# Performance work log

Hardware: AMD Instinct MI355X
Metric: run time of the kernel (lower is better)

Reference implementation:

```python
import jax, jax.numpy as jnp
import numpy as np

# E2M1 (FP4) representable magnitudes and rounding midpoints
LEVELS = jnp.array([0.0, 0.5, 1.0, 1.5, 2.0, 3.0, 4.0, 6.0], dtype=jnp.float32)
BOUNDS = jnp.array([0.25, 0.75, 1.25, 1.75, 2.5, 3.5, 5.0], dtype=jnp.float32)
E2M1_MAX = 6.0
EPS = 1e-12


def e2m1_block_quant_dequant(x, block_size):
    """Block-wise E2M1 fake-quantization along the last dim.

    Per block of `block_size` elements: scale = absmax / 6.0, then
    round-to-nearest onto the E2M1 grid {0,.5,1,1.5,2,3,4,6} (signed)
    and dequantize. Returns (dequantized x, per-block scales).
    """
    shape = x.shape
    nb = shape[-1] // block_size
    xb = x.reshape(*shape[:-1], nb, block_size)
    amax = jnp.max(jnp.abs(xb), axis=-1, keepdims=True)          # [..., nb, 1]
    scale = jnp.maximum(amax / E2M1_MAX, EPS)
    v = xb / scale
    mag = jnp.abs(v)
    # nearest E2M1 level: count how many rounding boundaries |v| exceeds
    idx = jnp.sum((mag[..., None] > BOUNDS).astype(jnp.int32), axis=-1)
    q = jnp.sign(v) * LEVELS[idx] * scale                        # dequantized
    return q.reshape(shape), scale[..., 0]


def setup_inputs() -> dict:
    key = jax.random.key(0)
    k1, k2, k3 = jax.random.split(key, 3)
    x = jax.random.normal(k1, (8, 1500, 1280), dtype=jnp.float32)
    weight = jax.random.normal(k2, (5120, 1280), dtype=jnp.float32) * 0.02
    bias = jax.random.normal(k3, (5120,), dtype=jnp.float32) * 0.01
    return {"x": x, "weight": weight, "bias": bias}


def reference(x, weight, bias):
    # activation quant (block_size_act = 32, along feature dim)
    x_q, _ = e2m1_block_quant_dequant(x, 32)
    # weight quant (block_size_w = 32, along in_features dim)
    w_q, scale_w = e2m1_block_quant_dequant(weight, 32)
    # F.linear: x @ W^T + b
    out = jnp.einsum('bsi,oi->bso', x_q, w_q) + bias
    return (out, scale_w)
```

## Files before the change

kernel.cpp:

```cpp
#include <hip/hip_runtime.h>
#include <hip/hip_fp16.h>


typedef _Float16 f16;
typedef _Float16 f16x8 __attribute__((ext_vector_type(8)));
typedef float f32x4 __attribute__((ext_vector_type(4)));

#define M_ROWS 12000
#define M_PAD  12032
#define N_COLS 5120
#define K_DIM  1280
#define KB     40
#define NT     20
#define NTN    20

#define BAR()   asm volatile("s_barrier" ::: "memory")
#define LGKM0() asm volatile("s_waitcnt lgkmcnt(0)" ::: "memory")
#define GLDS(gp, lp) __builtin_amdgcn_global_load_lds( \
    (const __attribute__((address_space(1))) unsigned*)(gp), \
    (__attribute__((address_space(3))) unsigned*)(lp), 16, 0, 0)

__device__ __forceinline__ float e2m1_level(float a) {
    float lv;
    if (a > 2.5f)       lv = (a > 3.5f) ? ((a > 5.0f) ? 6.0f : 4.0f) : 3.0f;
    else if (a > 1.25f) lv = (a > 1.75f) ? 2.0f : 1.5f;
    else                lv = (a > 0.75f) ? 1.0f : ((a > 0.25f) ? 0.5f : 0.0f);
    return lv;
}

__global__ __launch_bounds__(256) void quant_x_kernel(const float* __restrict__ x,
                                                      f16* __restrict__ xq) {
    int t = blockIdx.x * blockDim.x + threadIdx.x;
    int row = t / 160;
    int c8  = t % 160;
    f16x8 o;
    if (row < M_ROWS) {
        const float* p = x + (size_t)row * K_DIM + c8 * 8;
        float v[8];
        *(float4*)&v[0] = *(const float4*)p;
        *(float4*)&v[4] = *(const float4*)(p + 4);
        float am = 0.0f;
        #pragma unroll
        for (int i = 0; i < 8; ++i) am = fmaxf(am, fabsf(v[i]));
        am = fmaxf(am, __shfl_xor(am, 1));
        am = fmaxf(am, __shfl_xor(am, 2));
        float scale = fmaxf(am / 6.0f, 1e-12f);
        #pragma unroll
        for (int i = 0; i < 8; ++i) {
            float tq = v[i] / scale;
            float q  = copysignf(e2m1_level(fabsf(tq)), tq) * scale;
            o[i] = (f16)q;
        }
    } else {
        #pragma unroll
        for (int i = 0; i < 8; ++i) o[i] = (f16)0.0f;
    }
    *(f16x8*)(xq + (size_t)row * K_DIM + c8 * 8) = o;
}

__global__ __launch_bounds__(256) void quant_w_kernel(const float* __restrict__ w,
                                                      f16* __restrict__ wq,
                                                      float* __restrict__ scale_out) {
    int t = blockIdx.x * blockDim.x + threadIdx.x;
    int row = t / 160;
    int c8  = t % 160;
    const float* p = w + (size_t)row * K_DIM + c8 * 8;
    float v[8];
    *(float4*)&v[0] = *(const float4*)p;
    *(float4*)&v[4] = *(const float4*)(p + 4);
    float am = 0.0f;
    #pragma unroll
    for (int i = 0; i < 8; ++i) am = fmaxf(am, fabsf(v[i]));
    am = fmaxf(am, __shfl_xor(am, 1));
    am = fmaxf(am, __shfl_xor(am, 2));
    float scale = fmaxf(am / 6.0f, 1e-12f);
    if ((t & 3) == 0) scale_out[row * KB + (c8 >> 2)] = scale;
    f16x8 o;
    #pragma unroll
    for (int i = 0; i < 8; ++i) {
        float tq = v[i] / scale;
        float q  = copysignf(e2m1_level(fabsf(tq)), tq) * scale;
        o[i] = (f16)q;
    }
    *(f16x8*)(wq + (size_t)row * K_DIM + c8 * 8) = o;
}


__device__ __forceinline__ void stage_half(const f16* __restrict__ g, f16* l, int tid) {
    #pragma unroll
    for (int s = 0; s < 2; ++s) {
        int j = s * 512 + tid;
        int r = j >> 3;
        int c = (j & 7) ^ (r & 7);
        GLDS(g + (size_t)r * K_DIM + c * 8, l + (size_t)j * 8);
    }
}

template<bool STAGE, int VMN>
__device__ __forceinline__ void tile_body(f16* Ab, f16* Bb,
                                          const f16* gA2, const f16* gB2,
                                          f32x4 (&acc)[8][4],
                                          int tid, int l15, const int (&swz)[2],
                                          int wr, int wc) {
    f16x8 a0[4][2], a1[4][2], b0[2][2], b1[2][2];
    const int arow0 = wr * 128 + l15;
    const int brow0 = wc * 64 + l15;

    #pragma unroll
    for (int fm = 0; fm < 4; ++fm) {
        a0[fm][0] = *(const f16x8*)&Ab[(arow0 + fm * 16) * 64 + swz[0]];
        a0[fm][1] = *(const f16x8*)&Ab[(arow0 + fm * 16) * 64 + swz[1]];
    }
    #pragma unroll
    for (int fn = 0; fn < 2; ++fn) {
        b0[fn][0] = *(const f16x8*)&Bb[(brow0 + fn * 16) * 64 + swz[0]];
        b0[fn][1] = *(const f16x8*)&Bb[(brow0 + fn * 16) * 64 + swz[1]];
    }
    #pragma unroll
    for (int fn = 0; fn < 2; ++fn) {
        b1[fn][0] = *(const f16x8*)&Bb[(brow0 + 32 + fn * 16) * 64 + swz[0]];
        b1[fn][1] = *(const f16x8*)&Bb[(brow0 + 32 + fn * 16) * 64 + swz[1]];
    }
    BAR();
    __builtin_amdgcn_s_setprio(1);
    #pragma unroll
    for (int fm = 0; fm < 4; ++fm)
        #pragma unroll
        for (int fn = 0; fn < 2; ++fn) {
            acc[fm][fn] = __builtin_amdgcn_mfma_f32_16x16x32_f16(a0[fm][0], b0[fn][0], acc[fm][fn], 0, 0, 0);
            acc[fm][fn] = __builtin_amdgcn_mfma_f32_16x16x32_f16(a0[fm][1], b0[fn][1], acc[fm][fn], 0, 0, 0);
        }
    __builtin_amdgcn_s_setprio(0);
    BAR();

    __builtin_amdgcn_s_setprio(1);
    #pragma unroll
    for (int fm = 0; fm < 4; ++fm)
        #pragma unroll
        for (int fn = 0; fn < 2; ++fn) {
            acc[fm][fn + 2] = __builtin_amdgcn_mfma_f32_16x16x32_f16(a0[fm][0], b1[fn][0], acc[fm][fn + 2], 0, 0, 0);
            acc[fm][fn + 2] = __builtin_amdgcn_mfma_f32_16x16x32_f16(a0[fm][1], b1[fn][1], acc[fm][fn + 2], 0, 0, 0);
        }
    __builtin_amdgcn_s_setprio(0);
    LGKM0();
    BAR();

    #pragma unroll
    for (int fm = 0; fm < 4; ++fm) {
        a1[fm][0] = *(const f16x8*)&Ab[(arow0 + 64 + fm * 16) * 64 + swz[0]];
        a1[fm][1] = *(const f16x8*)&Ab[(arow0 + 64 + fm * 16) * 64 + swz[1]];
    }
    if (STAGE) {
        stage_half(gB2, Bb, tid);
        stage_half(gB2 + 128 * K_DIM, Bb + 8192, tid);
    }
    BAR();
    __builtin_amdgcn_s_setprio(1);
    #pragma unroll
    for (int fm = 0; fm < 4; ++fm)
        #pragma unroll
        for (int fn = 0; fn < 2; ++fn) {
            acc[fm + 4][fn + 2] = __builtin_amdgcn_mfma_f32_16x16x32_f16(a1[fm][0], b1[fn][0], acc[fm + 4][fn + 2], 0, 0, 0);
            acc[fm + 4][fn + 2] = __builtin_amdgcn_mfma_f32_16x16x32_f16(a1[fm][1], b1[fn][1], acc[fm + 4][fn + 2], 0, 0, 0);
        }
    __builtin_amdgcn_s_setprio(0);
    LGKM0();
    BAR();

    if (STAGE) {
        stage_half(gA2, Ab, tid);
        stage_half(gA2 + 128 * K_DIM, Ab + 8192, tid);
    }
    BAR();
    __builtin_amdgcn_s_setprio(1);
    #pragma unroll
    for (int fm = 0; fm < 4; ++fm)
        #pragma unroll
        for (int fn = 0; fn < 2; ++fn) {
            acc[fm + 4][fn] = __builtin_amdgcn_mfma_f32_16x16x32_f16(a1[fm][0], b0[fn][0], acc[fm + 4][fn], 0, 0, 0);
            acc[fm + 4][fn] = __builtin_amdgcn_mfma_f32_16x16x32_f16(a1[fm][1], b0[fn][1], acc[fm + 4][fn], 0, 0, 0);
        }
    __builtin_amdgcn_s_setprio(0);
    if (VMN == 8)      asm volatile("s_waitcnt vmcnt(8)" ::: "memory");
    else if (VMN == 0) asm volatile("s_waitcnt vmcnt(0)" ::: "memory");
    BAR();
}

__global__ __launch_bounds__(512, 2) void gemm_kernel(const f16* __restrict__ A,
                                                      const f16* __restrict__ B,
                                                      const float* __restrict__ bias,
                                                      float* __restrict__ C) {
    extern __shared__ f16 sm[];
    int mt = blockIdx.x / NTN;
    int nt = blockIdx.x % NTN;

    int tid  = threadIdx.x;
    int lane = tid & 63;
    int wid  = tid >> 6;
    int wr   = wid >> 2;
    int wc   = wid & 3;
    int l15  = lane & 15;

    int swz[2] = { (((lane >> 4)    ) ^ (lane & 7)) * 8,
                   (((lane >> 4) + 4) ^ (lane & 7)) * 8 };

    const f16* gAb = A + (size_t)(mt * 256) * K_DIM;
    const f16* gBb = B + (size_t)(nt * 256) * K_DIM;

    f16* A0 = sm;
    f16* B0 = sm + 16384;
    f16* A1 = sm + 32768;
    f16* B1 = sm + 49152;

    f32x4 acc[8][4] = {};

    stage_half(gAb,                A0, tid);
    stage_half(gAb + 128 * K_DIM,  A0 + 8192, tid);
    stage_half(gBb,                B0, tid);
    stage_half(gBb + 128 * K_DIM,  B0 + 8192, tid);
    stage_half(gAb + 64,               A1, tid);
    stage_half(gAb + 64 + 128 * K_DIM, A1 + 8192, tid);
    stage_half(gBb + 64,               B1, tid);
    stage_half(gBb + 64 + 128 * K_DIM, B1 + 8192, tid);
    asm volatile("s_waitcnt vmcnt(8)" ::: "memory");
    BAR();

    #pragma unroll 2
    for (int t = 0; t < NT - 2; ++t) {
        f16* Ab = (t & 1) ? A1 : A0;
        f16* Bb = (t & 1) ? B1 : B0;
        tile_body<true, 8>(Ab, Bb, gAb + (t + 2) * 64, gBb + (t + 2) * 64,
                           acc, tid, l15, swz, wr, wc);
    }
    tile_body<false, 0>(A0, B0, gAb, gBb, acc, tid, l15, swz, wr, wc);
    tile_body<false, -1>(A1, B1, gAb, gBb, acc, tid, l15, swz, wr, wc);

    int crow0 = mt * 256 + wr * 128;
    int ccol  = nt * 256 + wc * 64 + l15;
    float bz[4];
    #pragma unroll
    for (int fn = 0; fn < 4; ++fn) bz[fn] = bias[ccol + fn * 16];

    #pragma unroll
    for (int fm = 0; fm < 8; ++fm) {
        #pragma unroll
        for (int j = 0; j < 4; ++j) {
            int row = crow0 + fm * 16 + (lane >> 4) * 4 + j;
            if (row < M_ROWS) {
                float* cp = C + (size_t)row * N_COLS + ccol;
                #pragma unroll
                for (int fn = 0; fn < 4; ++fn)
                    cp[fn * 16] = acc[fm][fn][j] + bz[fn];
            }
        }
    }
}

extern "C" void kernel_launch(void* const* d_in, const int* in_sizes, int n_in,
                              void* d_out, int out_size, void* d_ws, size_t ws_size,
                              hipStream_t stream) {
    const float* x      = (const float*)d_in[0];
    const float* weight = (const float*)d_in[1];
    const float* bias   = (const float*)d_in[2];
    float* out     = (float*)d_out;
    float* scale_w = (float*)d_out + (size_t)M_ROWS * N_COLS;

    f16* xq = (f16*)d_ws;
    f16* wq = (f16*)((char*)d_ws + (size_t)M_PAD * K_DIM * sizeof(f16));

    (void)hipFuncSetAttribute((const void*)gemm_kernel,
                              hipFuncAttributeMaxDynamicSharedMemorySize, 131072);

    {
        int threads = M_PAD * (K_DIM / 8);
        quant_x_kernel<<<threads / 256, 256, 0, stream>>>(x, xq);
    }
    {
        int threads = N_COLS * (K_DIM / 8);
        quant_w_kernel<<<threads / 256, 256, 0, stream>>>(weight, wq, scale_w);
    }
    {
        int grid = (M_PAD / 256) * (N_COLS / 256);
        gemm_kernel<<<grid, 512, 131072, stream>>>(xq, wq, bias, out);
    }
}
```

Before: 209.8 us.

## Prefetch next tile's LDS fragments into registers and cut barriers per K-tile

Restructures the GEMM main loop so the A0/B0 fragments for the next K-tile are read from LDS into a double-buffered register set at the end of the current tile. MFMA blocks now interleave with LDS reads without barriers between them. Staging of both A and B for tile t+2 is merged into one point after a single barrier, which lowers barriers per tile from about six to two. The cost is more VGPR pressure from the doubled fragment registers, which could cause spills or limit occupancy under launch_bounds(512,2).

```diff
diff --git a/kernel.cpp b/kernel.cpp
--- a/kernel.cpp
+++ b/kernel.cpp
@@ -96,65 +96,54 @@
     }
 }
 
-template<bool STAGE, int VMN>
-__device__ __forceinline__ void tile_body(f16* Ab, f16* Bb,
+template<int PAR, bool STAGE, int VM, bool READNEXT>
+__device__ __forceinline__ void tile_body(f16* Xa, f16* Xb,
+                                          const f16* Na, const f16* Nb,
                                           const f16* gA2, const f16* gB2,
+                                          f16x8 (&a0)[2][4][2], f16x8 (&b0)[2][2][2],
                                           f32x4 (&acc)[8][4],
-                                          int tid, int l15, const int (&swz)[2],
-                                          int wr, int wc) {
-    f16x8 a0[4][2], a1[4][2], b0[2][2], b1[2][2];
-    const int arow0 = wr * 128 + l15;
-    const int brow0 = wc * 64 + l15;
+                                          int tid, int arow0, int brow0,
+                                          const int (&swz)[2]) {
+    f16x8 b1[2][2], a1[4][2];
+
+    #pragma unroll
+    for (int fn = 0; fn < 2; ++fn) {
+        b1[fn][0] = *(const f16x8*)&Xb[(brow0 + 32 + fn * 16) * 64 + swz[0]];
+        b1[fn][1] = *(const f16x8*)&Xb[(brow0 + 32 + fn * 16) * 64 + swz[1]];
+    }
+    __builtin_amdgcn_s_setprio(1);
+    #pragma unroll
+    for (int fm = 0; fm < 4; ++fm)
+        #pragma unroll
+        for (int fn = 0; fn < 2; ++fn) {
+            acc[fm][fn] = __builtin_amdgcn_mfma_f32_16x16x32_f16(a0[PAR][fm][0], b0[PAR][fn][0], acc[fm][fn], 0, 0, 0);
+            acc[fm][fn] = __builtin_amdgcn_mfma_f32_16x16x32_f16(a0[PAR][fm][1], b0[PAR][fn][1], acc[fm][fn], 0, 0, 0);
+        }
+    __builtin_amdgcn_s_setprio(0);
 
     #pragma unroll
     for (int fm = 0; fm < 4; ++fm) {
-        a0[fm][0] = *(const f16x8*)&Ab[(arow0 + fm * 16) * 64 + swz[0]];
-        a0[fm][1] = *(const f16x8*)&Ab[(arow0 + fm * 16) * 64 + swz[1]];
-    }
-    #pragma unroll
-    for (int fn = 0; fn < 2; ++fn) {
-        b0[fn][0] = *(const f16x8*)&Bb[(brow0 + fn * 16) * 64 + swz[0]];
-        b0[fn][1] = *(const f16x8*)&Bb[(brow0 + fn * 16) * 64 + swz[1]];
-    }
-    #pragma unroll
-    for (int fn = 0; fn < 2; ++fn) {
-        b1[fn][0] = *(const f16x8*)&Bb[(brow0 + 32 + fn * 16) * 64 + swz[0]];
-        b1[fn][1] = *(const f16x8*)&Bb[(brow0 + 32 + fn * 16) * 64 + swz[1]];
-    }
-    BAR();
-    __builtin_amdgcn_s_setprio(1);
-    #pragma unroll
-    for (int fm = 0; fm < 4; ++fm)
-        #pragma unroll
-        for (int fn = 0; fn < 2; ++fn) {
-            acc[fm][fn] = __builtin_amdgcn_mfma_f32_16x16x32_f16(a0[fm][0], b0[fn][0], acc[fm][fn], 0, 0, 0);
-            acc[fm][fn] = __builtin_amdgcn_mfma_f32_16x16x32_f16(a0[fm][1], b0[fn][1], acc[fm][fn], 0, 0, 0);
-        }
-    __builtin_amdgcn_s_setprio(0);
-    BAR();
-
-    __builtin_amdgcn_s_setprio(1);
-    #pragma unroll
-    for (int fm = 0; fm < 4; ++fm)
-        #pragma unroll
-        for (int fn = 0; fn < 2; ++fn) {
-            acc[fm][fn + 2] = __builtin_amdgcn_mfma_f32_16x16x32_f16(a0[fm][0], b1[fn][0], acc[fm][fn + 2], 0, 0, 0);
-            acc[fm][fn + 2] = __builtin_amdgcn_mfma_f32_16x16x32_f16(a0[fm][1], b1[fn][1], acc[fm][fn + 2], 0, 0, 0);
-        }
-    __builtin_amdgcn_s_setprio(0);
-    LGKM0();
-    BAR();
-
-    #pragma unroll
-    for (int fm = 0; fm < 4; ++fm) {
-        a1[fm][0] = *(const f16x8*)&Ab[(arow0 + 64 + fm * 16) * 64 + swz[0]];
-        a1[fm][1] = *(const f16x8*)&Ab[(arow0 + 64 + fm * 16) * 64 + swz[1]];
-    }
+        a1[fm][0] = *(const f16x8*)&Xa[(arow0 + 64 + fm * 16) * 64 + swz[0]];
+        a1[fm][1] = *(const f16x8*)&Xa[(arow0 + 64 + fm * 16) * 64 + swz[1]];
+    }
+    __builtin_amdgcn_s_setprio(1);
+    #pragma unroll
+    for (int fm = 0; fm < 4; ++fm)
+        #pragma unroll
+        for (int fn = 0; fn < 2; ++fn) {
+            acc[fm][fn + 2] = __builtin_amdgcn_mfma_f32_16x16x32_f16(a0[PAR][fm][0], b1[fn][0], acc[fm][fn + 2], 0, 0, 0);
+            acc[fm][fn + 2] = __builtin_amdgcn_mfma_f32_16x16x32_f16(a0[PAR][fm][1], b1[fn][1], acc[fm][fn + 2], 0, 0, 0);
+        }
+    __builtin_amdgcn_s_setprio(0);
+
     if (STAGE) {
-        stage_half(gB2, Bb, tid);
-        stage_half(gB2 + 128 * K_DIM, Bb + 8192, tid);
-    }
-    BAR();
+        LGKM0();
+        BAR();
+        stage_half(gA2,               Xa,        tid);
+        stage_half(gA2 + 128 * K_DIM, Xa + 8192, tid);
+        stage_half(gB2,               Xb,        tid);
+        stage_half(gB2 + 128 * K_DIM, Xb + 8192, tid);
+    }
     __builtin_amdgcn_s_setprio(1);
     #pragma unroll
     for (int fm = 0; fm < 4; ++fm)
@@ -164,26 +153,31 @@
             acc[fm + 4][fn + 2] = __builtin_amdgcn_mfma_f32_16x16x32_f16(a1[fm][1], b1[fn][1], acc[fm + 4][fn + 2], 0, 0, 0);
         }
     __builtin_amdgcn_s_setprio(0);
-    LGKM0();
-    BAR();
-
-    if (STAGE) {
-        stage_half(gA2, Ab, tid);
-        stage_half(gA2 + 128 * K_DIM, Ab + 8192, tid);
-    }
-    BAR();
-    __builtin_amdgcn_s_setprio(1);
-    #pragma unroll
-    for (int fm = 0; fm < 4; ++fm)
-        #pragma unroll
-        for (int fn = 0; fn < 2; ++fn) {
-            acc[fm + 4][fn] = __builtin_amdgcn_mfma_f32_16x16x32_f16(a1[fm][0], b0[fn][0], acc[fm + 4][fn], 0, 0, 0);
-            acc[fm + 4][fn] = __builtin_amdgcn_mfma_f32_16x16x32_f16(a1[fm][1], b0[fn][1], acc[fm + 4][fn], 0, 0, 0);
-        }
-    __builtin_amdgcn_s_setprio(0);
-    if (VMN == 8)      asm volatile("s_waitcnt vmcnt(8)" ::: "memory");
-    else if (VMN == 0) asm volatile("s_waitcnt vmcnt(0)" ::: "memory");
-    BAR();
+
+    if (READNEXT) {
+        if (VM == 8)  asm volatile("s_waitcnt vmcnt(8)" ::: "memory");
+        else          asm volatile("s_waitcnt vmcnt(0)" ::: "memory");
+        BAR();
+        #pragma unroll
+        for (int fm = 0; fm < 4; ++fm) {
+            a0[1 - PAR][fm][0] = *(const f16x8*)&Na[(arow0 + fm * 16) * 64 + swz[0]];
+            a0[1 - PAR][fm][1] = *(const f16x8*)&Na[(arow0 + fm * 16) * 64 + swz[1]];
+        }
+        #pragma unroll
+        for (int fn = 0; fn < 2; ++fn) {
+            b0[1 - PAR][fn][0] = *(const f16x8*)&Nb[(brow0 + fn * 16) * 64 + swz[0]];
+            b0[1 - PAR][fn][1] = *(const f16x8*)&Nb[(brow0 + fn * 16) * 64 + swz[1]];
+        }
+    }
+    __builtin_amdgcn_s_setprio(1);
+    #pragma unroll
+    for (int fm = 0; fm < 4; ++fm)
+        #pragma unroll
+        for (int fn = 0; fn < 2; ++fn) {
+            acc[fm + 4][fn] = __builtin_amdgcn_mfma_f32_16x16x32_f16(a1[fm][0], b0[PAR][fn][0], acc[fm + 4][fn], 0, 0, 0);
+            acc[fm + 4][fn] = __builtin_amdgcn_mfma_f32_16x16x32_f16(a1[fm][1], b0[PAR][fn][1], acc[fm + 4][fn], 0, 0, 0);
+        }
+    __builtin_amdgcn_s_setprio(0);
 }
 
 __global__ __launch_bounds__(512, 2) void gemm_kernel(const f16* __restrict__ A,
@@ -203,6 +197,8 @@
 
     int swz[2] = { (((lane >> 4)    ) ^ (lane & 7)) * 8,
                    (((lane >> 4) + 4) ^ (lane & 7)) * 8 };
+    int arow0 = wr * 128 + l15;
+    int brow0 = wc * 64 + l15;
 
     const f16* gAb = A + (size_t)(mt * 256) * K_DIM;
     const f16* gBb = B + (size_t)(nt * 256) * K_DIM;
@@ -213,27 +209,43 @@
     f16* B1 = sm + 49152;
 
     f32x4 acc[8][4] = {};
-
-    stage_half(gAb,                A0, tid);
-    stage_half(gAb + 128 * K_DIM,  A0 + 8192, tid);
-    stage_half(gBb,                B0, tid);
-    stage_half(gBb + 128 * K_DIM,  B0 + 8192, tid);
-    stage_half(gAb + 64,               A1, tid);
+    f16x8 a0[2][4][2];
+    f16x8 b0[2][2][2];
+
+    stage_half(gAb,               A0,        tid);
+    stage_half(gAb + 128 * K_DIM, A0 + 8192, tid);
+    stage_half(gBb,               B0,        tid);
+    stage_half(gBb + 128 * K_DIM, B0 + 8192, tid);
+    stage_half(gAb + 64,               A1,        tid);
     stage_half(gAb + 64 + 128 * K_DIM, A1 + 8192, tid);
-    stage_half(gBb + 64,               B1, tid);
+    stage_half(gBb + 64,               B1,        tid);
     stage_half(gBb + 64 + 128 * K_DIM, B1 + 8192, tid);
     asm volatile("s_waitcnt vmcnt(8)" ::: "memory");
     BAR();
-
-    #pragma unroll 2
-    for (int t = 0; t < NT - 2; ++t) {
-        f16* Ab = (t & 1) ? A1 : A0;
-        f16* Bb = (t & 1) ? B1 : B0;
-        tile_body<true, 8>(Ab, Bb, gAb + (t + 2) * 64, gBb + (t + 2) * 64,
-                           acc, tid, l15, swz, wr, wc);
-    }
-    tile_body<false, 0>(A0, B0, gAb, gBb, acc, tid, l15, swz, wr, wc);
-    tile_body<false, -1>(A1, B1, gAb, gBb, acc, tid, l15, swz, wr, wc);
+    #pragma unroll
+    for (int fm = 0; fm < 4; ++fm) {
+        a0[0][fm][0] = *(const f16x8*)&A0[(arow0 + fm * 16) * 64 + swz[0]];
+        a0[0][fm][1] = *(const f16x8*)&A0[(arow0 + fm * 16) * 64 + swz[1]];
+    }
+    #pragma unroll
+    for (int fn = 0; fn < 2; ++fn) {
+        b0[0][fn][0] = *(const f16x8*)&B0[(brow0 + fn * 16) * 64 + swz[0]];
+        b0[0][fn][1] = *(const f16x8*)&B0[(brow0 + fn * 16) * 64 + swz[1]];
+    }
+
+    for (int tt = 0; tt < 9; ++tt) {
+        int t0 = 2 * tt;
+        tile_body<0, true, 8, true>(A0, B0, A1, B1,
+                                    gAb + (t0 + 2) * 64, gBb + (t0 + 2) * 64,
+                                    a0, b0, acc, tid, arow0, brow0, swz);
+        tile_body<1, true, 8, true>(A1, B1, A0, B0,
+                                    gAb + (t0 + 3) * 64, gBb + (t0 + 3) * 64,
+                                    a0, b0, acc, tid, arow0, brow0, swz);
+    }
+    tile_body<0, false, 0, true>(A0, B0, A1, B1, gAb, gBb,
+                                 a0, b0, acc, tid, arow0, brow0, swz);
+    tile_body<1, false, -1, false>(A1, B1, A0, B0, gAb, gBb,
+                                   a0, b0, acc, tid, arow0, brow0, swz);
 
     int crow0 = mt * 256 + wr * 128;
     int ccol  = nt * 256 + wc * 64 + l15;
```

Result: slower. 243.0 us (+15.8%).
